# Kernel optimization log

Hardware: AMD Instinct MI355X
Metric: run time of the kernel (lower is better)

The kernel has to match this reference:

```python
import jax, jax.numpy as jnp
import numpy as np

L_TEACHER, L_STUDENT = 36, 28
B, H, S, D = 1, 16, 1024, 128
TEMPERATURE = 1.0

def _stride_prior_logits(student, teacher):
    # init: logits[i, j] = -|j - i*teacher/student|
    i = np.arange(student)[:, None].astype(np.float32)
    j = np.arange(teacher)[None, :].astype(np.float32)
    return jnp.asarray(-np.abs(j - i * teacher / student), dtype=jnp.float32)

def setup_inputs() -> dict:
    key = jax.random.key(0)
    k1, k2 = jax.random.split(key)
    ks = jax.random.normal(k1, (L_TEACHER, B, H, S, D), dtype=jnp.float32)
    vs = jax.random.normal(k2, (L_TEACHER, B, H, S, D), dtype=jnp.float32)
    logits = _stride_prior_logits(L_STUDENT, L_TEACHER)
    return {"ks": ks, "vs": vs, "attn_logits_k": logits, "attn_logits_v": logits}

def reference(ks, vs, attn_logits_k, attn_logits_v):
    # softmax over teacher-layer dim, then weighted sum across the 36 layers
    attn_k = jax.nn.softmax(attn_logits_k / TEMPERATURE, axis=-1)  # [28, 36]
    attn_v = jax.nn.softmax(attn_logits_v / TEMPERATURE, axis=-1)  # [28, 36]
    ks_pooled = jnp.einsum('lbhsd,ml->mbhsd', ks, attn_k)  # [28, B, H, S, D]
    vs_pooled = jnp.einsum('lbhsd,ml->mbhsd', vs, attn_v)  # [28, B, H, S, D]
    return (ks_pooled, vs_pooled)
```

## Files before the change

kernel.cpp:

```cpp
#include <hip/hip_runtime.h>
#include <cstddef>


constexpr int LT = 36;
constexpr int LS = 28;
constexpr int N2 = 1048576;
constexpr int TILE = 64;
constexpr int TPT = N2 / TILE;
constexpr int NTILES = 2 * TPT;
constexpr int TPB = 256;
constexpr int NBLOCKS = 1024;
constexpr int W_TENSOR_STRIDE = 9 * LS * 4;

typedef __attribute__((ext_vector_type(4))) float f32x4;

__global__ __launch_bounds__(64) void softmax_kernel(
    const float* __restrict__ lgk, const float* __restrict__ lgv,
    float* __restrict__ ws)
{
    const int t = threadIdx.x;
    const int isv = t >> 5;
    const int m = t & 31;
    if (m >= LS) return;
    const float* row = (isv ? lgv : lgk) + m * LT;
    float mx = -3.4e38f;
    for (int l = 0; l < LT; ++l) mx = fmaxf(mx, row[l]);
    float s = 0.f;
    for (int l = 0; l < LT; ++l) s += expf(row[l] - mx);
    const float inv = 1.0f / s;
    float* o = ws + isv * W_TENSOR_STRIDE;
    for (int l = 0; l < LT; ++l)
        o[(l >> 2) * (LS * 4) + m * 4 + (l & 3)] = expf(row[l] - mx) * inv;
}

template<int LB>
__device__ __forceinline__ void do_lb(const float* wq,
                                      const float2 (*cur)[TILE],
                                      int lane, float2* acc)
{
    float2 d[4];
#pragma unroll
    for (int j = 0; j < 4; ++j) d[j] = cur[4 * LB + j][lane];

    f32x4 w0, w1, w2, w3, w4, w5, w6;
    asm volatile(
        "s_load_dwordx4 %0, %[b], %[o0]\n\t"
        "s_load_dwordx4 %1, %[b], %[o1]\n\t"
        "s_load_dwordx4 %2, %[b], %[o2]\n\t"
        "s_load_dwordx4 %3, %[b], %[o3]\n\t"
        "s_load_dwordx4 %4, %[b], %[o4]\n\t"
        "s_load_dwordx4 %5, %[b], %[o5]\n\t"
        "s_load_dwordx4 %6, %[b], %[o6]\n\t"
        "s_waitcnt lgkmcnt(0)"
        : "=s"(w0), "=s"(w1), "=s"(w2), "=s"(w3), "=s"(w4), "=s"(w5), "=s"(w6)
        : [b] "s"(wq),
          [o0] "i"(LB * 448 + 0),  [o1] "i"(LB * 448 + 16),
          [o2] "i"(LB * 448 + 32), [o3] "i"(LB * 448 + 48),
          [o4] "i"(LB * 448 + 64), [o5] "i"(LB * 448 + 80),
          [o6] "i"(LB * 448 + 96));

    const f32x4 W[7] = {w0, w1, w2, w3, w4, w5, w6};
#pragma unroll
    for (int k = 0; k < 7; ++k) {
        acc[k].x = fmaf(W[k].x, d[0].x, acc[k].x);
        acc[k].y = fmaf(W[k].x, d[0].y, acc[k].y);
        acc[k].x = fmaf(W[k].y, d[1].x, acc[k].x);
        acc[k].y = fmaf(W[k].y, d[1].y, acc[k].y);
        acc[k].x = fmaf(W[k].z, d[2].x, acc[k].x);
        acc[k].y = fmaf(W[k].z, d[2].y, acc[k].y);
        acc[k].x = fmaf(W[k].w, d[3].x, acc[k].x);
        acc[k].y = fmaf(W[k].w, d[3].y, acc[k].y);
    }
}

__global__ __launch_bounds__(TPB) void pool_kernel(
    const float2* __restrict__ ks,
    const float2* __restrict__ vs,
    const float* __restrict__ ws,
    float2* __restrict__ out)
{
    __shared__ float2 smA[LT][TILE];
    __shared__ float2 smB[LT][TILE];

    const int tid  = threadIdx.x;
    const int wv   = tid >> 6;
    const int lane = tid & 63;
    const int wvu  = __builtin_amdgcn_readfirstlane(wv);
    const int m0   = 7 * wvu;

    const size_t lofs = (size_t)(lane >> 5) * N2 + (size_t)((lane & 31) << 1);

    auto stage = [&](float2 (*buf)[TILE], int t) {
        const float2* src = (t >= TPT) ? vs : ks;
        const size_t c0 = (size_t)(t & (TPT - 1)) * TILE;
        for (int i = wv; i < 18; i += 4) {
            const float2* g = src + (size_t)(2 * i) * N2 + c0 + lofs;
            __builtin_amdgcn_global_load_lds(
                (const __attribute__((address_space(1))) void*)g,
                (__attribute__((address_space(3))) void*)&buf[2 * i][0],
                16, 0, 0);
        }
    };

    int t = blockIdx.x;
    stage(smA, t);
    __syncthreads();

    float2 (*cur)[TILE] = smA;
    float2 (*nxt)[TILE] = smB;

    for (;;) {
        const int tn = t + NBLOCKS;
        const bool more = (tn < NTILES);

        if (more) stage(nxt, tn);

        if (more) asm volatile("s_waitcnt vmcnt(11)" ::: "memory");
        else      asm volatile("s_waitcnt vmcnt(7)"  ::: "memory");
        __builtin_amdgcn_sched_barrier(0);
        asm volatile("s_barrier" ::: "memory");

        const bool isv = (t >= TPT);
        const float* wq = ws + (isv ? W_TENSOR_STRIDE : 0) + m0 * 4;
        const size_t c0 = (size_t)(t & (TPT - 1)) * TILE;
        float2* dstb = out + (isv ? (size_t)LS * N2 : (size_t)0);

        float2 acc[7];
#pragma unroll
        for (int k = 0; k < 7; ++k) acc[k] = make_float2(0.f, 0.f);

        do_lb<0>(wq, cur, lane, acc);
        do_lb<1>(wq, cur, lane, acc);
        do_lb<2>(wq, cur, lane, acc);
        do_lb<3>(wq, cur, lane, acc);
        do_lb<4>(wq, cur, lane, acc);
        do_lb<5>(wq, cur, lane, acc);
        do_lb<6>(wq, cur, lane, acc);
        do_lb<7>(wq, cur, lane, acc);
        do_lb<8>(wq, cur, lane, acc);

#pragma unroll
        for (int k = 0; k < 7; ++k) {
            dstb[(size_t)(m0 + k) * N2 + c0 + lane] = acc[k];
        }

        if (!more) break;

        asm volatile("s_barrier" ::: "memory");

        t = tn;
        float2 (*tmp)[TILE] = cur; cur = nxt; nxt = tmp;
    }
}

extern "C" void kernel_launch(void* const* d_in, const int* in_sizes, int n_in,
                              void* d_out, int out_size, void* d_ws, size_t ws_size,
                              hipStream_t stream)
{
    const float2* ks  = (const float2*)d_in[0];
    const float2* vs  = (const float2*)d_in[1];
    const float* lgk  = (const float*)d_in[2];
    const float* lgv  = (const float*)d_in[3];
    float* ws = (float*)d_ws;
    float2* out = (float2*)d_out;

    hipLaunchKernelGGL(softmax_kernel, dim3(1), dim3(64), 0, stream,
                       lgk, lgv, ws);
    hipLaunchKernelGGL(pool_kernel, dim3(NBLOCKS), dim3(TPB), 0, stream,
                       ks, vs, ws, out);
}
```

Measured before the change: 238.4 us.

## Use single-wave blocks computing all 28 outputs per lane without barriers

The pooling kernel goes from 256-thread blocks, where four waves each produce 7 student layers on float2 data, to 64-thread blocks where one wave produces all 28 student layers for one float per lane. Each block stages all 36 teacher layers of a 64-float tile into LDS with nine 16-byte direct-to-LDS loads per lane. Because only one wave uses the LDS tile, the block barriers are removed and plain vmcnt waits are enough. The grid doubles to 2048 blocks. In exchange, each wave holds 28 accumulators and issues four times more scalar weight loads per element, and fewer waves per CU may fit under the LDS budget, which could reduce memory-latency hiding.

```diff
diff --git a/kernel.cpp b/kernel.cpp
--- a/kernel.cpp
+++ b/kernel.cpp
@@ -4,13 +4,12 @@
 
 constexpr int LT = 36;
 constexpr int LS = 28;
-constexpr int N2 = 1048576;
-constexpr int TILE = 64;
-constexpr int TPT = N2 / TILE;
+constexpr int NELEM = 2097152;
+constexpr int TILE_F = 64;
+constexpr int TPT = NELEM / TILE_F;
 constexpr int NTILES = 2 * TPT;
-constexpr int TPB = 256;
-constexpr int NBLOCKS = 1024;
-constexpr int W_TENSOR_STRIDE = 9 * LS * 4;
+constexpr int NBLOCKS = 2048;
+constexpr int W_STRIDE = 9 * LS * 4;
 
 typedef __attribute__((ext_vector_type(4))) float f32x4;
 
@@ -28,20 +27,15 @@
     float s = 0.f;
     for (int l = 0; l < LT; ++l) s += expf(row[l] - mx);
     const float inv = 1.0f / s;
-    float* o = ws + isv * W_TENSOR_STRIDE;
+    float* o = ws + isv * W_STRIDE;
     for (int l = 0; l < LT; ++l)
         o[(l >> 2) * (LS * 4) + m * 4 + (l & 3)] = expf(row[l] - mx) * inv;
 }
 
-template<int LB>
-__device__ __forceinline__ void do_lb(const float* wq,
-                                      const float2 (*cur)[TILE],
-                                      int lane, float2* acc)
+template<int LB, int G>
+__device__ __forceinline__ void do_grp(const float* wq, const float d[4],
+                                       float* acc)
 {
-    float2 d[4];
-#pragma unroll
-    for (int j = 0; j < 4; ++j) d[j] = cur[4 * LB + j][lane];
-
     f32x4 w0, w1, w2, w3, w4, w5, w6;
     asm volatile(
         "s_load_dwordx4 %0, %[b], %[o0]\n\t"
@@ -54,60 +48,72 @@
         "s_waitcnt lgkmcnt(0)"
         : "=s"(w0), "=s"(w1), "=s"(w2), "=s"(w3), "=s"(w4), "=s"(w5), "=s"(w6)
         : [b] "s"(wq),
-          [o0] "i"(LB * 448 + 0),  [o1] "i"(LB * 448 + 16),
-          [o2] "i"(LB * 448 + 32), [o3] "i"(LB * 448 + 48),
-          [o4] "i"(LB * 448 + 64), [o5] "i"(LB * 448 + 80),
-          [o6] "i"(LB * 448 + 96));
+          [o0] "i"(LB * 448 + G * 112 + 0),
+          [o1] "i"(LB * 448 + G * 112 + 16),
+          [o2] "i"(LB * 448 + G * 112 + 32),
+          [o3] "i"(LB * 448 + G * 112 + 48),
+          [o4] "i"(LB * 448 + G * 112 + 64),
+          [o5] "i"(LB * 448 + G * 112 + 80),
+          [o6] "i"(LB * 448 + G * 112 + 96));
 
     const f32x4 W[7] = {w0, w1, w2, w3, w4, w5, w6};
 #pragma unroll
     for (int k = 0; k < 7; ++k) {
-        acc[k].x = fmaf(W[k].x, d[0].x, acc[k].x);
-        acc[k].y = fmaf(W[k].x, d[0].y, acc[k].y);
-        acc[k].x = fmaf(W[k].y, d[1].x, acc[k].x);
-        acc[k].y = fmaf(W[k].y, d[1].y, acc[k].y);
-        acc[k].x = fmaf(W[k].z, d[2].x, acc[k].x);
-        acc[k].y = fmaf(W[k].z, d[2].y, acc[k].y);
-        acc[k].x = fmaf(W[k].w, d[3].x, acc[k].x);
-        acc[k].y = fmaf(W[k].w, d[3].y, acc[k].y);
+        float a = acc[7 * G + k];
+        a = fmaf(W[k].x, d[0], a);
+        a = fmaf(W[k].y, d[1], a);
+        a = fmaf(W[k].z, d[2], a);
+        a = fmaf(W[k].w, d[3], a);
+        acc[7 * G + k] = a;
     }
 }
 
-__global__ __launch_bounds__(TPB) void pool_kernel(
-    const float2* __restrict__ ks,
-    const float2* __restrict__ vs,
+template<int LB>
+__device__ __forceinline__ void do_lb(const float* wq,
+                                      const float (*cur)[TILE_F],
+                                      int lane, float* acc)
+{
+    float d[4];
+#pragma unroll
+    for (int j = 0; j < 4; ++j) d[j] = cur[4 * LB + j][lane];
+    do_grp<LB, 0>(wq, d, acc);
+    do_grp<LB, 1>(wq, d, acc);
+    do_grp<LB, 2>(wq, d, acc);
+    do_grp<LB, 3>(wq, d, acc);
+}
+
+__global__ __launch_bounds__(64) void pool_kernel(
+    const float* __restrict__ ks,
+    const float* __restrict__ vs,
     const float* __restrict__ ws,
-    float2* __restrict__ out)
+    float* __restrict__ out)
 {
-    __shared__ float2 smA[LT][TILE];
-    __shared__ float2 smB[LT][TILE];
+    __shared__ float smA[LT][TILE_F];
+    __shared__ float smB[LT][TILE_F];
 
-    const int tid  = threadIdx.x;
-    const int wv   = tid >> 6;
-    const int lane = tid & 63;
-    const int wvu  = __builtin_amdgcn_readfirstlane(wv);
-    const int m0   = 7 * wvu;
+    const int lane = threadIdx.x;
 
-    const size_t lofs = (size_t)(lane >> 5) * N2 + (size_t)((lane & 31) << 1);
+    const size_t lofs = (size_t)(lane >> 4) * NELEM + (size_t)((lane & 15) << 2);
 
-    auto stage = [&](float2 (*buf)[TILE], int t) {
-        const float2* src = (t >= TPT) ? vs : ks;
-        const size_t c0 = (size_t)(t & (TPT - 1)) * TILE;
-        for (int i = wv; i < 18; i += 4) {
-            const float2* g = src + (size_t)(2 * i) * N2 + c0 + lofs;
+    auto stage = [&](float (*buf)[TILE_F], int t) {
+        const float* src = (t >= TPT) ? vs : ks;
+        const size_t c0 = (size_t)(t & (TPT - 1)) * TILE_F;
+#pragma unroll
+        for (int i = 0; i < 9; ++i) {
+            const float* g = src + (size_t)(4 * i) * NELEM + c0 + lofs;
             __builtin_amdgcn_global_load_lds(
                 (const __attribute__((address_space(1))) void*)g,
-                (__attribute__((address_space(3))) void*)&buf[2 * i][0],
+                (__attribute__((address_space(3))) void*)&buf[4 * i][0],
                 16, 0, 0);
         }
     };
 
     int t = blockIdx.x;
     stage(smA, t);
-    __syncthreads();
+    asm volatile("s_waitcnt vmcnt(0)" ::: "memory");
 
-    float2 (*cur)[TILE] = smA;
-    float2 (*nxt)[TILE] = smB;
+    float (*cur)[TILE_F] = smA;
+    float (*nxt)[TILE_F] = smB;
 
     for (;;) {
         const int tn = t + NBLOCKS;
@@ -115,19 +121,18 @@
 
         if (more) stage(nxt, tn);
 
-        if (more) asm volatile("s_waitcnt vmcnt(11)" ::: "memory");
-        else      asm volatile("s_waitcnt vmcnt(7)"  ::: "memory");
+        if (more) asm volatile("s_waitcnt vmcnt(37)" ::: "memory");
+        else      asm volatile("s_waitcnt vmcnt(28)" ::: "memory");
         __builtin_amdgcn_sched_barrier(0);
-        asm volatile("s_barrier" ::: "memory");
 
         const bool isv = (t >= TPT);
-        const float* wq = ws + (isv ? W_TENSOR_STRIDE : 0) + m0 * 4;
-        const size_t c0 = (size_t)(t & (TPT - 1)) * TILE;
-        float2* dstb = out + (isv ? (size_t)LS * N2 : (size_t)0);
+        const float* wq = ws + (isv ? W_STRIDE : 0);
+        const size_t c0 = (size_t)(t & (TPT - 1)) * TILE_F;
+        float* dstb = out + (isv ? (size_t)LS * NELEM : (size_t)0);
 
-        float2 acc[7];
+        float acc[LS];
 #pragma unroll
-        for (int k = 0; k < 7; ++k) acc[k] = make_float2(0.f, 0.f);
+        for (int m = 0; m < LS; ++m) acc[m] = 0.f;
 
         do_lb<0>(wq, cur, lane, acc);
         do_lb<1>(wq, cur, lane, acc);
@@ -140,16 +145,12 @@
         do_lb<8>(wq, cur, lane, acc);
 
 #pragma unroll
-        for (int k = 0; k < 7; ++k) {
-            dstb[(size_t)(m0 + k) * N2 + c0 + lane] = acc[k];
-        }
+        for (int m = 0; m < LS; ++m)
+            dstb[(size_t)m * NELEM + c0 + lane] = acc[m];
 
         if (!more) break;
-
-        asm volatile("s_barrier" ::: "memory");
-
         t = tn;
-        float2 (*tmp)[TILE] = cur; cur = nxt; nxt = tmp;
+        float (*tmp)[TILE_F] = cur; cur = nxt; nxt = tmp;
     }
 }
 
@@ -157,15 +158,15 @@
                               void* d_out, int out_size, void* d_ws, size_t ws_size,
                               hipStream_t stream)
 {
-    const float2* ks  = (const float2*)d_in[0];
-    const float2* vs  = (const float2*)d_in[1];
-    const float* lgk  = (const float*)d_in[2];
-    const float* lgv  = (const float*)d_in[3];
-    float* ws = (float*)d_ws;
-    float2* out = (float2*)d_out;
+    const float* ks  = (const float*)d_in[0];
+    const float* vs  = (const float*)d_in[1];
+    const float* lgk = (const float*)d_in[2];
+    const float* lgv = (const float*)d_in[3];
+    float* ws  = (float*)d_ws;
+    float* out = (float*)d_out;
 
     hipLaunchKernelGGL(softmax_kernel, dim3(1), dim3(64), 0, stream,
                        lgk, lgv, ws);
-    hipLaunchKernelGGL(pool_kernel, dim3(NBLOCKS), dim3(TPB), 0, stream,
+    hipLaunchKernelGGL(pool_kernel, dim3(NBLOCKS), dim3(64), 0, stream,
                        ks, vs, ws, out);
 }
```

Result: slower. 244.5 us (+2.6%).
